# Kernel tuning notes

Measured on AMD Instinct MI355X. Metric: run time of the kernel, lower is better.

## Reference

```python
import jax, jax.numpy as jnp
import numpy as np
from jax import lax

N, D = 8, 32            # batch, map_depth
S = 2                   # belief_downsample_factor
HS, WS = 512, 512       # semantic map resolution
H, W = HS // S, WS // S # belief resolution (256, 256)
K = 7                   # motion_kernel_size
KK = K * K
HID = 64                # motion_hidden_size
A = 256                 # action_embedding_size


def _conv(x, w, b, pad, dil=1):
    # x: NCHW, w: OIHW
    y = lax.conv_general_dilated(
        x, w, window_strides=(1, 1), padding=[(pad, pad), (pad, pad)],
        rhs_dilation=(dil, dil), dimension_numbers=('NCHW', 'OIHW', 'NCHW'))
    return y + b[None, :, None, None]


def _unfold_index():
    # Reproduces nn.Unfold([K,K]) applied to ConstantPad2d(K//2, -1)(arange image).
    # Result flattened in (ki*K+kj, i, j) order, matching col2im flatten order.
    pad = K // 2
    img = np.arange(H * W, dtype=np.int64).reshape(H, W)
    imgp = np.pad(img, ((pad, pad), (pad, pad)), constant_values=-1)
    idx = np.empty((K, K, H, W), dtype=np.int64)
    for ki in range(K):
        for kj in range(K):
            idx[ki, kj] = imgp[ki:ki + H, kj:kj + W]
    return idx.reshape(-1)  # (K*K*H*W,)

_IDX = _unfold_index()
_VALID = _IDX >= 0
_IDX_SAFE = np.where(_VALID, _IDX, 0)


def _scatter_logsumexp(src, idx, num_segments):
    # src: (B, M) with -inf marking invalid entries; idx: (M,) shared across B.
    def one(s):
        mx = jax.ops.segment_max(s, idx, num_segments=num_segments)          # (P,)
        g = mx[idx]                                                          # (M,)
        contrib = jnp.where(jnp.isneginf(s), 0.0,
                            jnp.exp(s - jnp.where(jnp.isfinite(g), g, 0.0)))
        sm = jax.ops.segment_sum(contrib, idx, num_segments=num_segments)    # (P,)
        return mx + jnp.log(jnp.where(jnp.isfinite(mx), sm, 1.0))
    return jax.vmap(one)(src)


def setup_inputs() -> dict:
    key = jax.random.key(0)
    ks = jax.random.split(key, 20)
    f32 = jnp.float32
    return {
        'log_belief': jax.random.normal(ks[0], (N, 1, H, W), f32),
        'semantic_map': jax.random.normal(ks[1], (N, D, HS, WS), f32),
        'action': jax.random.normal(ks[2], (N, A), f32),
        # Bottleneck(map_depth -> hidden -> map_depth, dilations [3,1])
        'w_in': jax.random.normal(ks[3], (HID, D, 1, 1), f32) * 0.1,
        'b_in': jnp.zeros((HID,), f32),
        'w_d3': jax.random.normal(ks[4], (HID, HID, 3, 3), f32) * 0.05,
        'b_d3': jnp.zeros((HID,), f32),
        'w_d1': jax.random.normal(ks[5], (HID, HID, 3, 3), f32) * 0.05,
        'b_d1': jnp.zeros((HID,), f32),
        'w_out': jax.random.normal(ks[6], (D, HID, 1, 1), f32) * 0.1,
        'b_out': jnp.zeros((D,), f32),
        # conv1x1: map_depth -> K*K
        'w_k': jax.random.normal(ks[7], (KK, D, 1, 1), f32) * 0.1,
        'b_k': jnp.zeros((KK,), f32),
        # DenseMlpBlock2: A -> hidden -> K*K
        'w_a1': jax.random.normal(ks[8], (A, HID), f32) * 0.05,
        'b_a1': jnp.zeros((HID,), f32),
        'w_a2': jax.random.normal(ks[9], (HID, KK), f32) * 0.05,
        'b_a2': jnp.zeros((KK,), f32),
    }


def reference(log_belief, semantic_map, action,
              w_in, b_in, w_d3, b_d3, w_d1, b_d1, w_out, b_out,
              w_k, b_k, w_a1, b_a1, w_a2, b_a2):
    # Dropout in eval mode -> identity. MaxPool2d(S, stride=S):
    x = lax.reduce_window(semantic_map, -jnp.inf, lax.max,
                          (1, 1, S, S), (1, 1, S, S), 'VALID')  # (N,D,H,W)
    # Bottleneck (conv1x1 -> dilated 3x3 convs -> conv1x1, residual)
    h = jax.nn.relu(_conv(x, w_in, b_in, 0))
    h = jax.nn.relu(_conv(h, w_d3, b_d3, 3, 3))
    h = jax.nn.relu(_conv(h, w_d1, b_d1, 1, 1))
    x2 = x + _conv(h, w_out, b_out, 0)
    # motion kernel logits over K*K taps per pixel
    motion = jax.nn.log_softmax(_conv(x2, w_k, b_k, 0), axis=1)   # (N,KK,H,W)
    lang = jax.nn.log_softmax(
        jax.nn.relu(action @ w_a1 + b_a1) @ w_a2 + b_a2, axis=1)  # (N,KK)
    log_kernel = jax.nn.log_softmax(motion + lang[:, :, None, None], axis=1)
    # propagate_belief: col2im + scatter_logsumexp (C=1, Cin=Cout=1)
    src = (log_belief + log_kernel).reshape(N, -1)                # (N, KK*H*W)
    idx = jnp.asarray(_IDX_SAFE)
    src = jnp.where(jnp.asarray(_VALID)[None, :], src, -jnp.inf)
    new_belief = _scatter_logsumexp(src, idx, H * W)              # (N, H*W)
    return new_belief.reshape(N, 1, H, W)
```

## Files before the change

kernel.cpp:

```cpp
#include <hip/hip_runtime.h>
#include <hip/hip_bf16.h>

typedef __hip_bfloat16 bf16;
typedef _Float16 fp16;
typedef __attribute__((ext_vector_type(8)))  short  short8;
typedef __attribute__((ext_vector_type(16))) float  floatx16;

#define HW 65536

__device__ __forceinline__ float b2f(bf16 v){ return __bfloat162float(v); }
__device__ __forceinline__ bf16  f2b(float v){ return __float2bfloat16(v); }
__device__ __forceinline__ unsigned short f2bu(float v){
  union { bf16 h; unsigned short u; } cv; cv.h = __float2bfloat16(v); return cv.u;
}
__device__ __forceinline__ float bu2f(unsigned short u){
  union { unsigned u; float f; } cv; cv.u = ((unsigned)u) << 16; return cv.f;
}
__device__ __forceinline__ unsigned short f2hu(float v){
  union { fp16 h; unsigned short u; } cv; cv.h = (fp16)v; return cv.u;
}
__device__ __forceinline__ float hu2f(unsigned short u){
  union { fp16 h; unsigned short u; } cv; cv.u = u; return (float)cv.h;
}

__global__ __launch_bounds__(256) void setup_kernel(
    const float* __restrict__ w_d3, const float* __restrict__ w_d1,
    bf16* __restrict__ wb3, bf16* __restrict__ wb1,
    const float* __restrict__ action,
    const float* __restrict__ w_a1, const float* __restrict__ b_a1,
    const float* __restrict__ w_a2, const float* __restrict__ b_a2,
    float* __restrict__ lang){
  int b = blockIdx.x;
  if (b < 288){
    const float* w = (b < 144) ? w_d3 : w_d1;
    bf16* wb = (b < 144) ? wb3 : wb1;
    int i = (b < 144 ? b : b - 144)*256 + threadIdx.x;
    if (i >= 36864) return;
    int j    = i & 7;
    int gran = i >> 3;
    int oc   = gran & 63;
    int rest = gran >> 6;
    int half = rest & 1;
    int ks   = (rest >> 1) & 3;
    int t    = rest >> 3;
    int e  = ks*16 + half*8 + j;
    int ki = t / 3, kj = t - ki*3;
    wb[i] = f2b(w[(oc*64 + e)*9 + ki*3 + kj]);
  } else {
    int n = b - 288;
    int t = threadIdx.x;
    __shared__ float part[256];
    __shared__ float hid[64];
    int d = t & 63, q = t >> 6;
    const float* ar = action + n*256;
    float a = 0.f;
    #pragma unroll 8
    for (int i = q*64; i < q*64 + 64; i++) a += ar[i]*w_a1[i*64 + d];
    part[t] = a;
    __syncthreads();
    if (t < 64)
      hid[t] = fmaxf(b_a1[t] + part[t] + part[64+t] + part[128+t] + part[192+t], 0.f);
    __syncthreads();
    if (t < 49){
      float l = b_a2[t];
      #pragma unroll 8
      for (int j2 = 0; j2 < 64; j2++) l += hid[j2]*w_a2[j2*49 + t];
      lang[n*49 + t] = l;
    }
  }
}

__global__ __launch_bounds__(256) void pool_in_kernel(
    const float* __restrict__ sm, const float* __restrict__ w_in,
    const float* __restrict__ b_in, fp16* __restrict__ x, bf16* __restrict__ h1){
  int p = blockIdx.x*256 + threadIdx.x;
  int n = p >> 16; int ij = p & 65535; int i = ij >> 8; int j = ij & 255;
  const float* smn = sm + ((long)n << 23);
  float xv[32];
  #pragma unroll
  for (int d = 0; d < 32; d++){
    long base = ((long)(d*512 + 2*i) << 9) + 2*j;
    float2 p0 = *reinterpret_cast<const float2*>(smn + base);
    float2 p1 = *reinterpret_cast<const float2*>(smn + base + 512);
    xv[d] = fmaxf(fmaxf(p0.x, p0.y), fmaxf(p1.x, p1.y));
  }
  unsigned xw[16];
  #pragma unroll
  for (int q = 0; q < 16; q++)
    xw[q] = ((unsigned)f2hu(xv[2*q+1]) << 16) | f2hu(xv[2*q]);
  uint4* xo = reinterpret_cast<uint4*>((char*)x + ((long)p << 6));
  #pragma unroll
  for (int q = 0; q < 4; q++)
    xo[q] = make_uint4(xw[4*q], xw[4*q+1], xw[4*q+2], xw[4*q+3]);
  unsigned ow[32];
  #pragma unroll 4
  for (int c = 0; c < 64; c += 2){
    float a0 = b_in[c], a1 = b_in[c+1];
    #pragma unroll
    for (int d = 0; d < 32; d++){
      a0 += xv[d]*w_in[c*32+d];
      a1 += xv[d]*w_in[(c+1)*32+d];
    }
    ow[c>>1] = ((unsigned)f2bu(fmaxf(a1,0.f)) << 16) | f2bu(fmaxf(a0,0.f));
  }
  uint4* ho = reinterpret_cast<uint4*>((char*)h1 + ((long)p << 7));
  #pragma unroll
  for (int q = 0; q < 8; q++)
    ho[q] = make_uint4(ow[4*q], ow[4*q+1], ow[4*q+2], ow[4*q+3]);
}

template<int DIL>
__global__ __launch_bounds__(256) void conv3x3_mfma(
    const bf16* __restrict__ hin, const bf16* __restrict__ wb,
    const float* __restrict__ bias, bf16* __restrict__ hout){
  constexpr int R = 16 + 2*DIL, C = 16 + 2*DIL, NPIX = R*C;
  __shared__ __align__(16) char tile[NPIX*128];
  int b = blockIdx.x;
  int n = b & 7; int tb = b >> 3;
  int i0 = (tb >> 4) << 4, j0 = (tb & 15) << 4;
  int tid = threadIdx.x;
  const bf16* hn = hin + ((long)n << 22);
  for (int s = tid; s < NPIX*8; s += 256){
    int pix = s >> 3, g = s & 7;
    int r = pix / C, c = pix - r*C;
    int gi = i0 - DIL + r, gj = j0 - DIL + c;
    uint4 v = make_uint4(0u,0u,0u,0u);
    if (gi >= 0 && gi < 256 && gj >= 0 && gj < 256)
      v = *reinterpret_cast<const uint4*>(hn + (((long)((gi<<8) + gj)) << 6) + (g<<3));
    *reinterpret_cast<uint4*>(tile + pix*128 + ((g ^ (pix & 7)) << 4)) = v;
  }
  __syncthreads();
  int lane = tid & 63, wv = tid >> 6;
  int l31 = lane & 31, half = lane >> 5;
  floatx16 acc[2][2];
  #pragma unroll
  for (int m2 = 0; m2 < 2; m2++){
    acc[m2][0] = (floatx16)(0.0f);
    acc[m2][1] = (floatx16)(0.0f);
  }
  int prr[2], pcc[2];
  #pragma unroll
  for (int m2 = 0; m2 < 2; m2++){
    int pidx = (wv*2 + m2)*32 + l31;
    prr[m2] = pidx >> 4; pcc[m2] = pidx & 15;
  }
  const char* wbc = reinterpret_cast<const char*>(wb);
  for (int t = 0; t < 9; t++){
    int ki = t / 3, kj = t - ki*3;
    int pp[2];
    #pragma unroll
    for (int m2 = 0; m2 < 2; m2++)
      pp[m2] = (prr[m2] + ki*DIL)*C + (pcc[m2] + kj*DIL);
    short8 bfr[4][2];
    #pragma unroll
    for (int ks = 0; ks < 4; ks++){
      #pragma unroll
      for (int nt = 0; nt < 2; nt++)
        bfr[ks][nt] = *reinterpret_cast<const short8*>(
            wbc + ((((t*4 + ks)*2 + half)*64 + nt*32 + l31) << 4));
    }
    #pragma unroll
    for (int ks = 0; ks < 4; ks++){
      #pragma unroll
      for (int m2 = 0; m2 < 2; m2++){
        short8 afrag = *reinterpret_cast<const short8*>(
            tile + pp[m2]*128 + (((ks*2 + half) ^ (pp[m2] & 7)) << 4));
        acc[m2][0] = __builtin_amdgcn_mfma_f32_32x32x16_bf16(afrag, bfr[ks][0], acc[m2][0], 0, 0, 0);
        acc[m2][1] = __builtin_amdgcn_mfma_f32_32x32x16_bf16(afrag, bfr[ks][1], acc[m2][1], 0, 0, 0);
      }
    }
  }
  float bv0 = bias[l31], bv1 = bias[32 + l31];
  bf16* ho = hout + ((long)n << 22);
  #pragma unroll
  for (int m2 = 0; m2 < 2; m2++){
    #pragma unroll
    for (int reg = 0; reg < 16; reg++){
      int row = (reg & 3) + 8*(reg >> 2) + 4*half;
      int pidx = (wv*2 + m2)*32 + row;
      int pr = pidx >> 4, pc = pidx & 15;
      long off = ((long)(((i0+pr)<<8) + (j0+pc))) << 6;
      ho[off + l31]      = f2b(fmaxf(acc[m2][0][reg] + bv0, 0.f));
      ho[off + 32 + l31] = f2b(fmaxf(acc[m2][1][reg] + bv1, 0.f));
    }
  }
}

__global__ __launch_bounds__(256) void out_motion_kernel(
    const bf16* __restrict__ h3, const fp16* __restrict__ x,
    const float* __restrict__ w_out, const float* __restrict__ b_out,
    const float* __restrict__ w_k, const float* __restrict__ b_k,
    const float* __restrict__ lang, fp16* __restrict__ lk){
  int p = blockIdx.x*256 + threadIdx.x;
  int n = p >> 16; int ij = p & 65535;
  float hv[64];
  const uint4* hp = reinterpret_cast<const uint4*>((const char*)h3 + ((long)p << 7));
  #pragma unroll
  for (int q = 0; q < 8; q++){
    uint4 u = hp[q];
    unsigned uu[4] = {u.x, u.y, u.z, u.w};
    #pragma unroll
    for (int k = 0; k < 4; k++){
      hv[q*8 + 2*k]   = bu2f((unsigned short)(uu[k] & 0xffffu));
      hv[q*8 + 2*k+1] = bu2f((unsigned short)(uu[k] >> 16));
    }
  }
  float o[32];
  const uint4* xp = reinterpret_cast<const uint4*>((const char*)x + ((long)p << 6));
  #pragma unroll
  for (int q = 0; q < 4; q++){
    uint4 u = xp[q];
    unsigned uu[4] = {u.x, u.y, u.z, u.w};
    #pragma unroll
    for (int k = 0; k < 4; k++){
      o[q*8 + 2*k]   = hu2f((unsigned short)(uu[k] & 0xffffu));
      o[q*8 + 2*k+1] = hu2f((unsigned short)(uu[k] >> 16));
    }
  }
  #pragma unroll 4
  for (int d = 0; d < 32; d++){
    float acc = b_out[d];
    #pragma unroll
    for (int e = 0; e < 64; e++) acc += hv[e]*w_out[d*64+e];
    o[d] += acc;
  }
  float lg[49]; float m = -1e30f;
  #pragma unroll 7
  for (int k = 0; k < 49; k++){
    float acc = b_k[k] + lang[n*49+k];
    #pragma unroll
    for (int d = 0; d < 32; d++) acc += o[d]*w_k[k*32+d];
    lg[k] = acc; m = fmaxf(m, acc);
  }
  float s = 0.f;
  #pragma unroll
  for (int k = 0; k < 49; k++) s += __expf(lg[k]-m);
  float lse = m + __logf(s);
  #pragma unroll
  for (int k = 0; k < 49; k++)
    lk[(long)n*49*HW + (long)k*HW + ij] = (fp16)(lg[k] - lse);
}

__global__ __launch_bounds__(256) void gather_lse_kernel(
    const float* __restrict__ lb, const fp16* __restrict__ lk, float* __restrict__ out){
  int b = blockIdx.x;
  int n = b & 7;
  int ij = ((b >> 3) << 8) | threadIdx.x;
  int i = ij >> 8; int j = ij & 255;
  const fp16* lkn = lk + (long)n*49*HW;
  float v[49]; float m = -1e30f;
  #pragma unroll
  for (int ki = 0; ki < 7; ki++){
    int h = i + 3 - ki;
    bool hok = (h >= 0 && h < 256);
    #pragma unroll
    for (int kj = 0; kj < 7; kj++){
      int w = j + 3 - kj;
      float val = -1e30f;
      if (hok && w >= 0 && w < 256){
        int q = h*256 + w;
        val = lb[n*HW + q] + (float)lkn[(ki*7+kj)*HW + q];
      }
      v[ki*7+kj] = val; m = fmaxf(m, val);
    }
  }
  float s = 0.f;
  #pragma unroll
  for (int t = 0; t < 49; t++) s += __expf(v[t]-m);
  out[n*HW + ij] = m + __logf(s);
}

extern "C" void kernel_launch(void* const* d_in, const int* in_sizes, int n_in,
                              void* d_out, int out_size, void* d_ws, size_t ws_size,
                              hipStream_t stream) {
  (void)in_sizes; (void)n_in; (void)out_size; (void)ws_size;
  const float* lb    = (const float*)d_in[0];
  const float* sm    = (const float*)d_in[1];
  const float* act   = (const float*)d_in[2];
  const float* w_in  = (const float*)d_in[3];
  const float* b_in  = (const float*)d_in[4];
  const float* w_d3  = (const float*)d_in[5];
  const float* b_d3  = (const float*)d_in[6];
  const float* w_d1  = (const float*)d_in[7];
  const float* b_d1  = (const float*)d_in[8];
  const float* w_out = (const float*)d_in[9];
  const float* b_out = (const float*)d_in[10];
  const float* w_k   = (const float*)d_in[11];
  const float* b_k   = (const float*)d_in[12];
  const float* w_a1  = (const float*)d_in[13];
  const float* b_a1  = (const float*)d_in[14];
  const float* w_a2  = (const float*)d_in[15];
  const float* b_a2  = (const float*)d_in[16];
  float* out = (float*)d_out;

  char* ws = (char*)d_ws;
  fp16*  x    = (fp16*) (ws + 0);
  bf16*  h1   = (bf16*) (ws + 67108864);
  bf16*  h2   = (bf16*) (ws + 134217728);
  fp16*  lk   = (fp16*) (ws + 134217728);
  float* lang = (float*)(ws + 236978176);
  bf16*  wb3  = (bf16*) (ws + 236979968);
  bf16*  wb1  = (bf16*) (ws + 237053696);

  setup_kernel<<<296, 256, 0, stream>>>(w_d3, w_d1, wb3, wb1,
                                        act, w_a1, b_a1, w_a2, b_a2, lang);
  pool_in_kernel<<<2048, 256, 0, stream>>>(sm, w_in, b_in, x, h1);
  conv3x3_mfma<3><<<2048, 256, 0, stream>>>(h1, wb3, b_d3, h2);
  conv3x3_mfma<1><<<2048, 256, 0, stream>>>(h2, wb1, b_d1, h1);
  out_motion_kernel<<<2048, 256, 0, stream>>>(h1, x, w_out, b_out,
                                              w_k, b_k, lang, lk);
  gather_lse_kernel<<<2048, 256, 0, stream>>>(lb, lk, out);
}
```

Before: 679.5 us.

## Fuse dilation-1 conv with output/motion head and merge setup into pool kernel

Fuses the second 3x3 conv with the 1x1 output conv and motion-kernel log-softmax. The conv result is staged in shared memory instead of going through a global h3 buffer, which removes one full write and read of the 64-channel activation. Weight columns are permuted so each lane writes packed bf16 pairs as 32-bit stores. Setup and pooling are merged into one launch to save a kernel launch. The fused kernel carries more register pressure, and the output head now runs inside the MFMA kernel's block shape, which may lower occupancy.

```diff
diff --git a/kernel.cpp b/kernel.cpp
--- a/kernel.cpp
+++ b/kernel.cpp
@@ -8,7 +8,6 @@
 
 #define HW 65536
 
-__device__ __forceinline__ float b2f(bf16 v){ return __bfloat162float(v); }
 __device__ __forceinline__ bf16  f2b(float v){ return __float2bfloat16(v); }
 __device__ __forceinline__ unsigned short f2bu(float v){
   union { bf16 h; unsigned short u; } cv; cv.h = __float2bfloat16(v); return cv.u;
@@ -23,90 +22,92 @@
   union { fp16 h; unsigned short u; } cv; cv.u = u; return (float)cv.h;
 }
 
-__global__ __launch_bounds__(256) void setup_kernel(
+__global__ __launch_bounds__(256) void setup_pool_kernel(
+    const float* __restrict__ sm, const float* __restrict__ w_in,
+    const float* __restrict__ b_in, fp16* __restrict__ x, bf16* __restrict__ h1,
     const float* __restrict__ w_d3, const float* __restrict__ w_d1,
     bf16* __restrict__ wb3, bf16* __restrict__ wb1,
     const float* __restrict__ action,
     const float* __restrict__ w_a1, const float* __restrict__ b_a1,
     const float* __restrict__ w_a2, const float* __restrict__ b_a2,
     float* __restrict__ lang){
-  int b = blockIdx.x;
-  if (b < 288){
-    const float* w = (b < 144) ? w_d3 : w_d1;
-    bf16* wb = (b < 144) ? wb3 : wb1;
-    int i = (b < 144 ? b : b - 144)*256 + threadIdx.x;
-    if (i >= 36864) return;
-    int j    = i & 7;
-    int gran = i >> 3;
-    int oc   = gran & 63;
-    int rest = gran >> 6;
-    int half = rest & 1;
-    int ks   = (rest >> 1) & 3;
-    int t    = rest >> 3;
-    int e  = ks*16 + half*8 + j;
-    int ki = t / 3, kj = t - ki*3;
-    wb[i] = f2b(w[(oc*64 + e)*9 + ki*3 + kj]);
+  int blk = blockIdx.x;
+  if (blk < 2048){
+    int p = blk*256 + threadIdx.x;
+    int n = p >> 16; int ij = p & 65535; int i = ij >> 8; int j = ij & 255;
+    const float* smn = sm + ((long)n << 23);
+    float xv[32];
+    #pragma unroll
+    for (int d = 0; d < 32; d++){
+      long base = ((long)(d*512 + 2*i) << 9) + 2*j;
+      float2 p0 = *reinterpret_cast<const float2*>(smn + base);
+      float2 p1 = *reinterpret_cast<const float2*>(smn + base + 512);
+      xv[d] = fmaxf(fmaxf(p0.x, p0.y), fmaxf(p1.x, p1.y));
+    }
+    unsigned xw[16];
+    #pragma unroll
+    for (int q = 0; q < 16; q++)
+      xw[q] = ((unsigned)f2hu(xv[2*q+1]) << 16) | f2hu(xv[2*q]);
+    uint4* xo = reinterpret_cast<uint4*>((char*)x + ((long)p << 6));
+    #pragma unroll
+    for (int q = 0; q < 4; q++)
+      xo[q] = make_uint4(xw[4*q], xw[4*q+1], xw[4*q+2], xw[4*q+3]);
+    unsigned ow[32];
+    #pragma unroll 4
+    for (int c = 0; c < 64; c += 2){
+      float a0 = b_in[c], a1 = b_in[c+1];
+      #pragma unroll
+      for (int d = 0; d < 32; d++){
+        a0 += xv[d]*w_in[c*32+d];
+        a1 += xv[d]*w_in[(c+1)*32+d];
+      }
+      ow[c>>1] = ((unsigned)f2bu(fmaxf(a1,0.f)) << 16) | f2bu(fmaxf(a0,0.f));
+    }
+    uint4* ho = reinterpret_cast<uint4*>((char*)h1 + ((long)p << 7));
+    #pragma unroll
+    for (int q = 0; q < 8; q++)
+      ho[q] = make_uint4(ow[4*q], ow[4*q+1], ow[4*q+2], ow[4*q+3]);
   } else {
-    int n = b - 288;
-    int t = threadIdx.x;
-    __shared__ float part[256];
-    __shared__ float hid[64];
-    int d = t & 63, q = t >> 6;
-    const float* ar = action + n*256;
-    float a = 0.f;
-    #pragma unroll 8
-    for (int i = q*64; i < q*64 + 64; i++) a += ar[i]*w_a1[i*64 + d];
-    part[t] = a;
-    __syncthreads();
-    if (t < 64)
-      hid[t] = fmaxf(b_a1[t] + part[t] + part[64+t] + part[128+t] + part[192+t], 0.f);
-    __syncthreads();
-    if (t < 49){
-      float l = b_a2[t];
+    int b = blk - 2048;
+    if (b < 288){
+      const float* w = (b < 144) ? w_d3 : w_d1;
+      bf16* wb = (b < 144) ? wb3 : wb1;
+      int i = (b < 144 ? b : b - 144)*256 + threadIdx.x;
+      if (i >= 36864) return;
+      int j    = i & 7;
+      int gran = i >> 3;
+      int col  = gran & 63;
+      int oc   = ((col & 31) << 1) | (col >> 5);
+      int rest = gran >> 6;
+      int half = rest & 1;
+      int ks   = (rest >> 1) & 3;
+      int t    = rest >> 3;
+      int e  = ks*16 + half*8 + j;
+      int ki = t / 3, kj = t - ki*3;
+      wb[i] = f2b(w[(oc*64 + e)*9 + ki*3 + kj]);
+    } else {
+      int n = b - 288;
+      int t = threadIdx.x;
+      __shared__ float part[256];
+      __shared__ float hid[64];
+      int d = t & 63, q = t >> 6;
+      const float* ar = action + n*256;
+      float a = 0.f;
       #pragma unroll 8
-      for (int j2 = 0; j2 < 64; j2++) l += hid[j2]*w_a2[j2*49 + t];
-      lang[n*49 + t] = l;
-    }
-  }
-}
-
-__global__ __launch_bounds__(256) void pool_in_kernel(
-    const float* __restrict__ sm, const float* __restrict__ w_in,
-    const float* __restrict__ b_in, fp16* __restrict__ x, bf16* __restrict__ h1){
-  int p = blockIdx.x*256 + threadIdx.x;
-  int n = p >> 16; int ij = p & 65535; int i = ij >> 8; int j = ij & 255;
-  const float* smn = sm + ((long)n << 23);
-  float xv[32];
-  #pragma unroll
-  for (int d = 0; d < 32; d++){
-    long base = ((long)(d*512 + 2*i) << 9) + 2*j;
-    float2 p0 = *reinterpret_cast<const float2*>(smn + base);
-    float2 p1 = *reinterpret_cast<const float2*>(smn + base + 512);
-    xv[d] = fmaxf(fmaxf(p0.x, p0.y), fmaxf(p1.x, p1.y));
-  }
-  unsigned xw[16];
-  #pragma unroll
-  for (int q = 0; q < 16; q++)
-    xw[q] = ((unsigned)f2hu(xv[2*q+1]) << 16) | f2hu(xv[2*q]);
-  uint4* xo = reinterpret_cast<uint4*>((char*)x + ((long)p << 6));
-  #pragma unroll
-  for (int q = 0; q < 4; q++)
-    xo[q] = make_uint4(xw[4*q], xw[4*q+1], xw[4*q+2], xw[4*q+3]);
-  unsigned ow[32];
-  #pragma unroll 4
-  for (int c = 0; c < 64; c += 2){
-    float a0 = b_in[c], a1 = b_in[c+1];
-    #pragma unroll
-    for (int d = 0; d < 32; d++){
-      a0 += xv[d]*w_in[c*32+d];
-      a1 += xv[d]*w_in[(c+1)*32+d];
-    }
-    ow[c>>1] = ((unsigned)f2bu(fmaxf(a1,0.f)) << 16) | f2bu(fmaxf(a0,0.f));
-  }
-  uint4* ho = reinterpret_cast<uint4*>((char*)h1 + ((long)p << 7));
-  #pragma unroll
-  for (int q = 0; q < 8; q++)
-    ho[q] = make_uint4(ow[4*q], ow[4*q+1], ow[4*q+2], ow[4*q+3]);
+      for (int i = q*64; i < q*64 + 64; i++) a += ar[i]*w_a1[i*64 + d];
+      part[t] = a;
+      __syncthreads();
+      if (t < 64)
+        hid[t] = fmaxf(b_a1[t] + part[t] + part[64+t] + part[128+t] + part[192+t], 0.f);
+      __syncthreads();
+      if (t < 49){
+        float l = b_a2[t];
+        #pragma unroll 8
+        for (int j2 = 0; j2 < 64; j2++) l += hid[j2]*w_a2[j2*49 + t];
+        lang[n*49 + t] = l;
+      }
+    }
+  }
 }
 
 template<int DIL>
@@ -170,7 +171,7 @@
       }
     }
   }
-  float bv0 = bias[l31], bv1 = bias[32 + l31];
+  float bv0 = bias[2*l31], bv1 = bias[2*l31+1];
   bf16* ho = hout + ((long)n << 22);
   #pragma unroll
   for (int m2 = 0; m2 < 2; m2++){
@@ -179,58 +180,135 @@
       int row = (reg & 3) + 8*(reg >> 2) + 4*half;
       int pidx = (wv*2 + m2)*32 + row;
       int pr = pidx >> 4, pc = pidx & 15;
-      long off = ((long)(((i0+pr)<<8) + (j0+pc))) << 6;
-      ho[off + l31]      = f2b(fmaxf(acc[m2][0][reg] + bv0, 0.f));
-      ho[off + 32 + l31] = f2b(fmaxf(acc[m2][1][reg] + bv1, 0.f));
-    }
-  }
-}
-
-__global__ __launch_bounds__(256) void out_motion_kernel(
-    const bf16* __restrict__ h3, const fp16* __restrict__ x,
+      int off = ((i0+pr)<<8) + (j0+pc);
+      unsigned pk = ((unsigned)f2bu(fmaxf(acc[m2][1][reg] + bv1, 0.f)) << 16)
+                  |  f2bu(fmaxf(acc[m2][0][reg] + bv0, 0.f));
+      *reinterpret_cast<unsigned*>((char*)ho + (((long)off) << 7) + (l31 << 2)) = pk;
+    }
+  }
+}
+
+__global__ __launch_bounds__(256) void conv1_out_kernel(
+    const bf16* __restrict__ hin, const bf16* __restrict__ wb,
+    const float* __restrict__ bias, const fp16* __restrict__ x,
     const float* __restrict__ w_out, const float* __restrict__ b_out,
     const float* __restrict__ w_k, const float* __restrict__ b_k,
     const float* __restrict__ lang, fp16* __restrict__ lk){
-  int p = blockIdx.x*256 + threadIdx.x;
-  int n = p >> 16; int ij = p & 65535;
-  float hv[64];
-  const uint4* hp = reinterpret_cast<const uint4*>((const char*)h3 + ((long)p << 7));
+  constexpr int DIL = 1, R = 18, C = 18, NPIX = R*C;
+  __shared__ __align__(16) char tile[NPIX*128];
+  int b = blockIdx.x;
+  int n = b & 7; int tb = b >> 3;
+  int i0 = (tb >> 4) << 4, j0 = (tb & 15) << 4;
+  int tid = threadIdx.x;
+  const bf16* hn = hin + ((long)n << 22);
+  for (int s = tid; s < NPIX*8; s += 256){
+    int pix = s >> 3, g = s & 7;
+    int r = pix / C, c = pix - r*C;
+    int gi = i0 - DIL + r, gj = j0 - DIL + c;
+    uint4 v = make_uint4(0u,0u,0u,0u);
+    if (gi >= 0 && gi < 256 && gj >= 0 && gj < 256)
+      v = *reinterpret_cast<const uint4*>(hn + (((long)((gi<<8) + gj)) << 6) + (g<<3));
+    *reinterpret_cast<uint4*>(tile + pix*128 + ((g ^ (pix & 7)) << 4)) = v;
+  }
+  __syncthreads();
+  int lane = tid & 63, wv = tid >> 6;
+  int l31 = lane & 31, half = lane >> 5;
+  floatx16 acc[2][2];
+  #pragma unroll
+  for (int m2 = 0; m2 < 2; m2++){
+    acc[m2][0] = (floatx16)(0.0f);
+    acc[m2][1] = (floatx16)(0.0f);
+  }
+  int prr[2], pcc[2];
+  #pragma unroll
+  for (int m2 = 0; m2 < 2; m2++){
+    int pidx = (wv*2 + m2)*32 + l31;
+    prr[m2] = pidx >> 4; pcc[m2] = pidx & 15;
+  }
+  const char* wbc = reinterpret_cast<const char*>(wb);
+  for (int t = 0; t < 9; t++){
+    int ki = t / 3, kj = t - ki*3;
+    int pp[2];
+    #pragma unroll
+    for (int m2 = 0; m2 < 2; m2++)
+      pp[m2] = (prr[m2] + ki)*C + (pcc[m2] + kj);
+    short8 bfr[4][2];
+    #pragma unroll
+    for (int ks = 0; ks < 4; ks++){
+      #pragma unroll
+      for (int nt = 0; nt < 2; nt++)
+        bfr[ks][nt] = *reinterpret_cast<const short8*>(
+            wbc + ((((t*4 + ks)*2 + half)*64 + nt*32 + l31) << 4));
+    }
+    #pragma unroll
+    for (int ks = 0; ks < 4; ks++){
+      #pragma unroll
+      for (int m2 = 0; m2 < 2; m2++){
+        short8 afrag = *reinterpret_cast<const short8*>(
+            tile + pp[m2]*128 + (((ks*2 + half) ^ (pp[m2] & 7)) << 4));
+        acc[m2][0] = __builtin_amdgcn_mfma_f32_32x32x16_bf16(afrag, bfr[ks][0], acc[m2][0], 0, 0, 0);
+        acc[m2][1] = __builtin_amdgcn_mfma_f32_32x32x16_bf16(afrag, bfr[ks][1], acc[m2][1], 0, 0, 0);
+      }
+    }
+  }
+  __syncthreads();
+  float bv0 = bias[2*l31], bv1 = bias[2*l31+1];
+  #pragma unroll
+  for (int m2 = 0; m2 < 2; m2++){
+    #pragma unroll
+    for (int reg = 0; reg < 16; reg++){
+      int row = (reg & 3) + 8*(reg >> 2) + 4*half;
+      int pidx = (wv*2 + m2)*32 + row;
+      unsigned pk = ((unsigned)f2bu(fmaxf(acc[m2][1][reg] + bv1, 0.f)) << 16)
+                  |  f2bu(fmaxf(acc[m2][0][reg] + bv0, 0.f));
+      *reinterpret_cast<unsigned*>(
+          tile + pidx*128 + ((((l31>>2) ^ (pidx & 7))) << 4) + ((l31 & 3) << 2)) = pk;
+    }
+  }
+  __syncthreads();
+  int pr = tid >> 4, pc = tid & 15;
+  int ij = ((i0 + pr) << 8) | (j0 + pc);
+  long p = ((long)n << 16) | ij;
+  float o[32];
+  { const uint4* xp = reinterpret_cast<const uint4*>((const char*)x + (p << 6));
+    #pragma unroll
+    for (int q = 0; q < 4; q++){
+      uint4 u = xp[q];
+      unsigned uu[4] = {u.x, u.y, u.z, u.w};
+      #pragma unroll
+      for (int k = 0; k < 4; k++){
+        o[q*8 + 2*k]   = hu2f((unsigned short)(uu[k] & 0xffffu));
+        o[q*8 + 2*k+1] = hu2f((unsigned short)(uu[k] >> 16));
+      }
+    }
+  }
+  #pragma unroll
+  for (int d = 0; d < 32; d++) o[d] += b_out[d];
   #pragma unroll
   for (int q = 0; q < 8; q++){
-    uint4 u = hp[q];
+    uint4 u = *reinterpret_cast<const uint4*>(tile + tid*128 + ((q ^ (tid & 7)) << 4));
     unsigned uu[4] = {u.x, u.y, u.z, u.w};
+    float hvv[8];
     #pragma unroll
     for (int k = 0; k < 4; k++){
-      hv[q*8 + 2*k]   = bu2f((unsigned short)(uu[k] & 0xffffu));
-      hv[q*8 + 2*k+1] = bu2f((unsigned short)(uu[k] >> 16));
-    }
-  }
-  float o[32];
-  const uint4* xp = reinterpret_cast<const uint4*>((const char*)x + ((long)p << 6));
-  #pragma unroll
-  for (int q = 0; q < 4; q++){
-    uint4 u = xp[q];
-    unsigned uu[4] = {u.x, u.y, u.z, u.w};
-    #pragma unroll
-    for (int k = 0; k < 4; k++){
-      o[q*8 + 2*k]   = hu2f((unsigned short)(uu[k] & 0xffffu));
-      o[q*8 + 2*k+1] = hu2f((unsigned short)(uu[k] >> 16));
-    }
-  }
-  #pragma unroll 4
-  for (int d = 0; d < 32; d++){
-    float acc = b_out[d];
-    #pragma unroll
-    for (int e = 0; e < 64; e++) acc += hv[e]*w_out[d*64+e];
-    o[d] += acc;
+      hvv[2*k]   = bu2f((unsigned short)(uu[k] & 0xffffu));
+      hvv[2*k+1] = bu2f((unsigned short)(uu[k] >> 16));
+    }
+    #pragma unroll
+    for (int d = 0; d < 32; d++){
+      float s = 0.f;
+      #pragma unroll
+      for (int cc = 0; cc < 8; cc++) s += hvv[cc]*w_out[d*64 + q*8 + cc];
+      o[d] += s;
+    }
   }
   float lg[49]; float m = -1e30f;
   #pragma unroll 7
   for (int k = 0; k < 49; k++){
-    float acc = b_k[k] + lang[n*49+k];
-    #pragma unroll
-    for (int d = 0; d < 32; d++) acc += o[d]*w_k[k*32+d];
-    lg[k] = acc; m = fmaxf(m, acc);
+    float acc2 = b_k[k] + lang[n*49+k];
+    #pragma unroll
+    for (int d = 0; d < 32; d++) acc2 += o[d]*w_k[k*32+d];
+    lg[k] = acc2; m = fmaxf(m, acc2);
   }
   float s = 0.f;
   #pragma unroll
@@ -296,18 +374,17 @@
   char* ws = (char*)d_ws;
   fp16*  x    = (fp16*) (ws + 0);
   bf16*  h1   = (bf16*) (ws + 67108864);
+  fp16*  lk   = (fp16*) (ws + 67108864);
   bf16*  h2   = (bf16*) (ws + 134217728);
-  fp16*  lk   = (fp16*) (ws + 134217728);
   float* lang = (float*)(ws + 236978176);
   bf16*  wb3  = (bf16*) (ws + 236979968);
   bf16*  wb1  = (bf16*) (ws + 237053696);
 
-  setup_kernel<<<296, 256, 0, stream>>>(w_d3, w_d1, wb3, wb1,
-                                        act, w_a1, b_a1, w_a2, b_a2, lang);
-  pool_in_kernel<<<2048, 256, 0, stream>>>(sm, w_in, b_in, x, h1);
+  setup_pool_kernel<<<2344, 256, 0, stream>>>(sm, w_in, b_in, x, h1,
+                                              w_d3, w_d1, wb3, wb1,
+                                              act, w_a1, b_a1, w_a2, b_a2, lang);
   conv3x3_mfma<3><<<2048, 256, 0, stream>>>(h1, wb3, b_d3, h2);
-  conv3x3_mfma<1><<<2048, 256, 0, stream>>>(h2, wb1, b_d1, h1);
-  out_motion_kernel<<<2048, 256, 0, stream>>>(h1, x, w_out, b_out,
-                                              w_k, b_k, lang, lk);
+  conv1_out_kernel<<<2048, 256, 0, stream>>>(h2, wb1, b_d1, x, w_out, b_out,
+                                             w_k, b_k, lang, lk);
   gather_lse_kernel<<<2048, 256, 0, stream>>>(lb, lk, out);
 }
```

Result: no change. 677.9 us (-0.2%).
